# Kernel optimization log

Measured on AMD Instinct MI355X. Metric: run time of the kernel, lower is better.

## Reference

```python
import jax, jax.numpy as jnp
import numpy as np
import math

G, H, C_IN, C_QK, C_VAL, C_OUT = 12, 8, 64, 32, 32, 64
ROPE_BASE = 10000.0


def platonic_linear(x, W):
    # x: [B, N, G*ci]; W: [G, co, ci] group-shared weights.
    # Equivariant linear via (cyclic stand-in) Cayley table: out[g] = sum_g' W[(g'-g)%G] x[g']
    B, N, _ = x.shape
    co, ci = W.shape[1], W.shape[2]
    idx = (jnp.arange(G)[None, :] - jnp.arange(G)[:, None]) % G  # [G_out, G_in]
    Wfull = W[idx]  # [G, G, co, ci]
    xg = x.reshape(B, N, G, ci)
    out = jnp.einsum('bngi,hgoi->bnho', xg, Wfull)
    return out.reshape(B, N, G * co)


def rms_norm(x, w):
    eps = jnp.finfo(x.dtype).eps
    var = jnp.mean(x * x, axis=-1, keepdims=True)
    return x * jax.lax.rsqrt(var + eps) * w


def rotate_pairs(x, cos, sin):
    # interleaved pair rotation; x: [..., d], cos/sin: [..., d//2]
    x1, x2 = x[..., ::2], x[..., 1::2]
    o1 = x1 * cos - x2 * sin
    o2 = x1 * sin + x2 * cos
    return jnp.stack([o1, o2], axis=-1).reshape(x.shape)


def sequence_rope(x, pos):
    # x: [B, N, GH, c_qk]; pos: [B, N] int
    half = C_QK // 2
    inv_freq = ROPE_BASE ** (-jnp.arange(0, half, dtype=jnp.float32) / half)
    ang = pos.astype(jnp.float32)[..., None] * inv_freq  # [B, N, half]
    cos, sin = jnp.cos(ang)[:, :, None, :], jnp.sin(ang)[:, :, None, :]
    return rotate_pairs(x, cos, sin)


def z_rotations():
    # stand-in group rotations: z-axis rotations by 2*pi*g/G, [G, 3, 3]
    th = 2.0 * jnp.pi * jnp.arange(G, dtype=jnp.float32) / G
    c, s, z, o = jnp.cos(th), jnp.sin(th), jnp.zeros(G), jnp.ones(G)
    R = jnp.stack([c, -s, z, s, c, z, z, z, o], axis=-1).reshape(G, 3, 3)
    return R


def platonic_rope(x, coords, freqs):
    # x: [B, N, G, H, c_qk]; coords: [B, N, 3]; freqs: [H, c_qk//2, 3]
    R = z_rotations()
    phase = jnp.einsum('bnd,gde,hfe->bnghf', coords, R, freqs)  # [B,N,G,H,half]
    return rotate_pairs(x, jnp.cos(phase), jnp.sin(phase))


def setup_inputs() -> dict:
    key = jax.random.key(0)
    ks = jax.random.split(key, 10)
    B, N = 2, 512
    feat_Q = jax.random.normal(ks[0], (B, N, G * C_IN), dtype=jnp.float32)
    coords_Q = jax.random.normal(ks[1], (B, N, 3), dtype=jnp.float32)
    sequence_idxs = jnp.sort(jax.random.randint(ks[2], (B, N), 0, 2048), axis=-1).astype(jnp.int32)
    s_in = 1.0 / math.sqrt(G * C_IN)
    s_o = 1.0 / math.sqrt(G * H * C_VAL)
    Wq = jax.random.normal(ks[3], (G, H * C_QK, C_IN), dtype=jnp.float32) * s_in
    Wk = jax.random.normal(ks[4], (G, H * C_QK, C_IN), dtype=jnp.float32) * s_in
    Wv = jax.random.normal(ks[5], (G, H * C_VAL, C_IN), dtype=jnp.float32) * s_in
    Wo = jax.random.normal(ks[6], (G, C_OUT, H * C_VAL), dtype=jnp.float32) * s_o
    q_norm_w = jnp.ones((C_QK,), dtype=jnp.float32)
    k_norm_w = jnp.ones((C_QK,), dtype=jnp.float32)
    platonic_freqs = jax.random.normal(ks[7], (H, C_QK // 2, 3), dtype=jnp.float32)  # freq_sigma=1.0
    return dict(feat_Q=feat_Q, coords_Q=coords_Q, Wq=Wq, Wk=Wk, Wv=Wv, Wo=Wo,
                q_norm_w=q_norm_w, k_norm_w=k_norm_w, platonic_freqs=platonic_freqs,
                sequence_idxs=sequence_idxs)


def reference(feat_Q, coords_Q, Wq, Wk, Wv, Wo, q_norm_w, k_norm_w, platonic_freqs, sequence_idxs):
    B, NQ, _ = feat_Q.shape
    q = platonic_linear(feat_Q, Wq).reshape(B, NQ, G * H, C_QK)
    k = platonic_linear(feat_Q, Wk).reshape(B, NQ, G * H, C_QK)
    v = platonic_linear(feat_Q, Wv).reshape(B, NQ, G * H, C_VAL)
    q = rms_norm(q, q_norm_w)
    k = rms_norm(k, k_norm_w)
    q = sequence_rope(q, sequence_idxs)
    k = sequence_rope(k, sequence_idxs)
    q = platonic_rope(q.reshape(B, NQ, G, H, C_QK), coords_Q, platonic_freqs).reshape(B, NQ, G * H, C_QK)
    k = platonic_rope(k.reshape(B, NQ, G, H, C_QK), coords_Q, platonic_freqs).reshape(B, NQ, G * H, C_QK)
    # attention over G*H heads, scale 1/sqrt(c_qk) (as in SDPA)
    qh = q.transpose(0, 2, 1, 3)  # [B, GH, NQ, d]
    kh = k.transpose(0, 2, 1, 3)
    vh = v.transpose(0, 2, 1, 3)
    scores = jnp.einsum('bhqd,bhkd->bhqk', qh, kh) / math.sqrt(C_QK)
    attn = jax.nn.softmax(scores, axis=-1)
    out = jnp.einsum('bhqk,bhkd->bhqd', attn, vh)
    out = out.transpose(0, 2, 1, 3).reshape(B, NQ, G * H * C_VAL)
    return platonic_linear(out, Wo)
```

## Files before the change

### kernel.cpp

```cpp
#include <hip/hip_runtime.h>
#include <math.h>

#define NG   12
#define NH   8
#define CIN  64
#define CQK  32
#define CVAL 32
#define COUT 64
#define NB   2
#define NN   512
#define NROWS (NB * NN)
#define GHH  (NG * NH)
#define DIN  (NG * CIN)
#define DQK  (GHH * CQK)
#define DOUT (NG * COUT)

typedef __attribute__((ext_vector_type(8))) short bf16x8;
typedef __attribute__((ext_vector_type(4))) float f32x4;
typedef unsigned short ushort_t;

#define SZU ((size_t)NROWS * DQK)

__device__ __forceinline__ ushort_t bf16_rne(float v) {
    unsigned u = __float_as_uint(v);
    return (ushort_t)((u + 0x7fffu + ((u >> 16) & 1u)) >> 16);
}

__global__ __launch_bounds__(256) void prep_kernel(
    const float* __restrict__ feat,
    const float* __restrict__ Wq, const float* __restrict__ Wk,
    const float* __restrict__ Wv,
    ushort_t* __restrict__ Xrh, ushort_t* __restrict__ Xrl,
    ushort_t* __restrict__ Wqh, ushort_t* __restrict__ Wql)
{
    const int bb = blockIdx.x;
    if (bb < 384) {
        const int t  = bb * 256 + threadIdx.x;
        const int mr  = t & 15;
        const int u   = t >> 4;
        const int kc  = u % 96;
        const int m16 = u / 96;
        const float* src = feat + (size_t)(m16 * 16 + mr) * DIN + kc * 8;
        float v[8];
        *(float4*)v       = *(const float4*)src;
        *(float4*)(v + 4) = *(const float4*)(src + 4);
        ushort_t h8[8] __attribute__((aligned(16)));
        ushort_t l8[8] __attribute__((aligned(16)));
        #pragma unroll
        for (int j = 0; j < 8; ++j) {
            ushort_t hb = bf16_rne(v[j]);
            float hf = __uint_as_float(((unsigned)hb) << 16);
            h8[j] = hb;
            l8[j] = bf16_rne(v[j] - hf);
        }
        const size_t dst = ((size_t)m16 * 96 + kc) * 128 + mr * 8;
        *(uint4*)(Xrh + dst) = *(const uint4*)h8;
        *(uint4*)(Xrl + dst) = *(const uint4*)l8;
    } else {
        const int zz = (bb - 384) / 96;
        const float* W = (zz == 0) ? Wq : (zz == 1) ? Wk : Wv;
        ushort_t* hi = Wqh + (size_t)zz * 196608;
        ushort_t* lo = Wql + (size_t)zz * 196608;
        const int t  = ((bb - 384) % 96) * 256 + threadIdx.x;
        const int kc = t & 7;
        const int o  = (t >> 3) & 255;
        const int gp = t >> 11;
        const float* src = W + ((size_t)(gp * 256 + o)) * 64 + kc * 8;
        float v[8];
        *(float4*)v       = *(const float4*)src;
        *(float4*)(v + 4) = *(const float4*)(src + 4);
        ushort_t h8[8] __attribute__((aligned(16)));
        ushort_t l8[8] __attribute__((aligned(16)));
        #pragma unroll
        for (int j = 0; j < 8; ++j) {
            ushort_t hb = bf16_rne(v[j]);
            float hf = __uint_as_float(((unsigned)hb) << 16);
            h8[j] = hb;
            l8[j] = bf16_rne(v[j] - hf);
        }
        const size_t dst = ((size_t)(gp * 16 + (o >> 4)) * 8 + kc) * 128 + (o & 15) * 8;
        *(uint4*)(hi + dst) = *(const uint4*)h8;
        *(uint4*)(lo + dst) = *(const uint4*)l8;
    }
}

__global__ __launch_bounds__(256) void wo_swz_kernel(
    const float* __restrict__ Wo, ushort_t* __restrict__ hi,
    ushort_t* __restrict__ lo)
{
    const int t  = blockIdx.x * 256 + threadIdx.x;
    const int kc = t & 31;
    const int o  = (t >> 5) & 63;
    const int gp = t >> 11;
    const float* src = Wo + ((size_t)(gp * 64 + o)) * 256 + kc * 8;
    float v[8];
    *(float4*)v       = *(const float4*)src;
    *(float4*)(v + 4) = *(const float4*)(src + 4);
    ushort_t h8[8] __attribute__((aligned(16)));
    ushort_t l8[8] __attribute__((aligned(16)));
    #pragma unroll
    for (int j = 0; j < 8; ++j) {
        ushort_t hb = bf16_rne(v[j]);
        float hf = __uint_as_float(((unsigned)hb) << 16);
        h8[j] = hb;
        l8[j] = bf16_rne(v[j] - hf);
    }
    const size_t dst = ((size_t)(gp * 4 + (o >> 4)) * 32 + kc) * 128 + (o & 15) * 8;
    *(uint4*)(hi + dst) = *(const uint4*)h8;
    *(uint4*)(lo + dst) = *(const uint4*)l8;
}

__global__ __launch_bounds__(256, 1) void qkv_mfma_kernel(
    const ushort_t* __restrict__ Xrh, const ushort_t* __restrict__ Xrl,
    const ushort_t* __restrict__ Wrh, const ushort_t* __restrict__ Wrl,
    float* __restrict__ qo, float* __restrict__ ko, float* __restrict__ vo)
{
    const int z = blockIdx.z;
    float* __restrict__ out = (z == 0) ? qo : (z == 1) ? ko : vo;
    const ushort_t* Wh = Wrh + (size_t)z * 196608;
    const ushort_t* Wl = Wrl + (size_t)z * 196608;
    const int m0 = blockIdx.y * 128;
    const int c0 = blockIdx.x * 128;
    const int hg = c0 >> 8;
    const int o0 = c0 & 255;
    const int tid  = threadIdx.x;
    const int lane = tid & 63;
    const int w    = tid >> 6;
    const int wm   = (w >> 1) * 64;
    const int wn   = (w & 1) * 64;
    const int lm   = lane & 15;
    const int lq   = lane >> 4;
    const int tA0  = (m0 + wm) >> 4;
    const int ct0  = (o0 + wn) >> 4;

    f32x4 acc[4][4];
    #pragma unroll
    for (int i = 0; i < 4; ++i)
        #pragma unroll
        for (int j = 0; j < 4; ++j) acc[i][j] = (f32x4)(0.0f);

    for (int ks = 0; ks < 24; ++ks) {
        const int g = ks >> 1;
        int gp = g - hg; if (gp < 0) gp += NG;
        bf16x8 ah[4], al[4], bh[4], bl[4];
        #pragma unroll
        for (int mt = 0; mt < 4; ++mt) {
            const size_t aoff = ((size_t)(tA0 + mt) * 96 + ks * 4 + lq) * 128 + lm * 8;
            ah[mt] = *(const bf16x8*)(Xrh + aoff);
            al[mt] = *(const bf16x8*)(Xrl + aoff);
        }
        const size_t bbase = ((size_t)(gp * 16 + ct0) * 8 + (ks & 1) * 4 + lq) * 128 + lm * 8;
        #pragma unroll
        for (int nt = 0; nt < 4; ++nt) {
            bh[nt] = *(const bf16x8*)(Wh + bbase + nt * 1024);
            bl[nt] = *(const bf16x8*)(Wl + bbase + nt * 1024);
        }
        #pragma unroll
        for (int mt = 0; mt < 4; ++mt)
            #pragma unroll
            for (int nt = 0; nt < 4; ++nt) {
                acc[mt][nt] = __builtin_amdgcn_mfma_f32_16x16x32_bf16(ah[mt], bh[nt], acc[mt][nt], 0, 0, 0);
                acc[mt][nt] = __builtin_amdgcn_mfma_f32_16x16x32_bf16(ah[mt], bl[nt], acc[mt][nt], 0, 0, 0);
                acc[mt][nt] = __builtin_amdgcn_mfma_f32_16x16x32_bf16(al[mt], bh[nt], acc[mt][nt], 0, 0, 0);
            }
    }
    #pragma unroll
    for (int mt = 0; mt < 4; ++mt)
        #pragma unroll
        for (int r = 0; r < 4; ++r) {
            float* dst = out + (size_t)(m0 + wm + mt * 16 + lq * 4 + r) * DQK + c0 + wn + lm;
            #pragma unroll
            for (int nt = 0; nt < 4; ++nt) dst[nt * 16] = acc[mt][nt][r];
        }
}

__global__ __launch_bounds__(256) void norm_rope_kernel(
    float* __restrict__ q, const float* __restrict__ kin,
    ushort_t* __restrict__ krh, ushort_t* __restrict__ krl,
    const float* __restrict__ coords,
    const int* __restrict__ seq,
    const float* __restrict__ qw,
    const float* __restrict__ kw,
    const float* __restrict__ pf)
{
    const int hid = blockIdx.x * 256 + threadIdx.x;
    const int gh = hid % GHH;
    const int bn = hid / GHH;
    const int g = gh >> 3;
    const int h = gh & 7;
    float* qp = q + (size_t)hid * CQK;
    const float* kp = kin + (size_t)hid * CQK;
    float xq[CQK], xk[CQK];
    #pragma unroll
    for (int u = 0; u < 8; ++u) *(float4*)(xq + 4 * u) = *(const float4*)(qp + 4 * u);
    #pragma unroll
    for (int u = 0; u < 8; ++u) *(float4*)(xk + 4 * u) = *(const float4*)(kp + 4 * u);

    float sq = 0.f, sk = 0.f;
    #pragma unroll
    for (int c = 0; c < CQK; ++c) { sq = fmaf(xq[c], xq[c], sq); sk = fmaf(xk[c], xk[c], sk); }
    const float eps = 1.1920928955078125e-07f;
    const float invq = rsqrtf(sq * (1.f / CQK) + eps);
    const float invk = rsqrtf(sk * (1.f / CQK) + eps);
    #pragma unroll
    for (int c = 0; c < CQK; ++c) { xq[c] *= invq * qw[c]; xk[c] *= invk * kw[c]; }

    const float pos = (float)seq[bn];
    const float cx = coords[bn * 3 + 0], cy = coords[bn * 3 + 1], cz = coords[bn * 3 + 2];
    float sg, cg;
    sincosf((float)g * 0.5235987755982988f, &sg, &cg);
    const float u0 = cg * cx + sg * cy;
    const float u1 = cg * cy - sg * cx;
    const float u2 = cz;

    #pragma unroll
    for (int f = 0; f < 16; ++f) {
        const float invf = exp2f(-(float)f * 0.8304820237218405f);
        const float* fr = pf + ((size_t)h * 16 + f) * 3;
        const float ang = fmaf(pos, invf, u0 * fr[0] + u1 * fr[1] + u2 * fr[2]);
        float sn, cs;
        sincosf(ang, &sn, &cs);
        float a1 = xq[2 * f], a2 = xq[2 * f + 1];
        xq[2 * f]     = a1 * cs - a2 * sn;
        xq[2 * f + 1] = a1 * sn + a2 * cs;
        float b1 = xk[2 * f], b2 = xk[2 * f + 1];
        xk[2 * f]     = b1 * cs - b2 * sn;
        xk[2 * f + 1] = b1 * sn + b2 * cs;
    }
    #pragma unroll
    for (int u = 0; u < 8; ++u) *(float4*)(qp + 4 * u) = *(const float4*)(xq + 4 * u);

    const int b = bn >> 9, n = bn & 511;
    const size_t kbase = (((size_t)(b * GHH + gh) * 32 + (n >> 4)) * 4) * 128 + (n & 15) * 8;
    #pragma unroll
    for (int kc = 0; kc < 4; ++kc) {
        ushort_t h8[8] __attribute__((aligned(16)));
        ushort_t l8[8] __attribute__((aligned(16)));
        #pragma unroll
        for (int j = 0; j < 8; ++j) {
            const float x = xk[kc * 8 + j];
            const ushort_t hb = bf16_rne(x);
            h8[j] = hb;
            l8[j] = bf16_rne(x - __uint_as_float(((unsigned)hb) << 16));
        }
        *(uint4*)(krh + kbase + kc * 128) = *(const uint4*)h8;
        *(uint4*)(krl + kbase + kc * 128) = *(const uint4*)l8;
    }
}

__global__ __launch_bounds__(256) void vpack_kernel(
    const float* __restrict__ v,
    ushort_t* __restrict__ vrh, ushort_t* __restrict__ vrl)
{
    const int t  = blockIdx.x * 256 + threadIdx.x;
    const int vd = t & 31;
    const int kc = (t >> 5) & 63;
    const int bg = t >> 11;
    const int b  = (bg >= GHH) ? 1 : 0;
    const int gh = bg - b * GHH;
    const float* src = v + (size_t)(b * 512 + kc * 8) * DQK + gh * 32 + vd;
    ushort_t h8[8] __attribute__((aligned(16)));
    ushort_t l8[8] __attribute__((aligned(16)));
    #pragma unroll
    for (int j = 0; j < 8; ++j) {
        const float x = src[j * DQK];
        const ushort_t hb = bf16_rne(x);
        h8[j] = hb;
        l8[j] = bf16_rne(x - __uint_as_float(((unsigned)hb) << 16));
    }
    const size_t dst = ((size_t)(bg * 2 + (vd >> 4)) * 64 + kc) * 128 + (vd & 15) * 8;
    *(uint4*)(vrh + dst) = *(const uint4*)h8;
    *(uint4*)(vrl + dst) = *(const uint4*)l8;
}

__global__ __launch_bounds__(256, 1) void attn_mfma_kernel(
    const float* __restrict__ q,
    const ushort_t* __restrict__ krh, const ushort_t* __restrict__ krl,
    const ushort_t* __restrict__ vrh, const ushort_t* __restrict__ vrl,
    ushort_t* __restrict__ aoh,
    ushort_t* __restrict__ aol)
{
    __shared__ __attribute__((aligned(16))) ushort_t Ps[128][72];

    const int gh    = blockIdx.x;
    const int chunk = blockIdx.y;
    const int b     = blockIdx.z;
    const size_t headoff = (size_t)b * NN * DQK + (size_t)gh * CQK;
    const size_t kvhead = (size_t)(b * GHH + gh) * 16384;
    const int tid  = threadIdx.x;
    const int lane = tid & 63;
    const int w    = tid >> 6;
    const int lm   = lane & 15;
    const int lq   = lane >> 4;
    const int qloc = w * 32;

    const float scale = 0.17677669529663687f;
    bf16x8 qh[2], ql[2];
    #pragma unroll
    for (int mt = 0; mt < 2; ++mt) {
        const int row = chunk * 128 + qloc + mt * 16 + lm;
        const float* qp = q + headoff + (size_t)row * DQK + lq * 8;
        float4 t0 = *(const float4*)qp;
        float4 t1 = *(const float4*)(qp + 4);
        float vals[8] = {t0.x, t0.y, t0.z, t0.w, t1.x, t1.y, t1.z, t1.w};
        short h8[8], l8[8];
        #pragma unroll
        for (int j = 0; j < 8; ++j) {
            float x = vals[j] * scale;
            ushort_t hb = bf16_rne(x);
            float hf = __uint_as_float(((unsigned)hb) << 16);
            h8[j] = (short)hb;
            l8[j] = (short)bf16_rne(x - hf);
        }
        qh[mt] = *(bf16x8*)h8;
        ql[mt] = *(bf16x8*)l8;
    }

    float lacc[2][4];
    f32x4 o[2][2];
    #pragma unroll
    for (int mt = 0; mt < 2; ++mt) {
        #pragma unroll
        for (int r = 0; r < 4; ++r) lacc[mt][r] = 0.f;
        o[mt][0] = (f32x4)(0.0f); o[mt][1] = (f32x4)(0.0f);
    }

    for (int j0 = 0; j0 < NN; j0 += 64) {
        f32x4 sf[2][4];
        #pragma unroll
        for (int nt = 0; nt < 4; ++nt) {
            const size_t kb = kvhead + ((size_t)(((j0 >> 4) + nt) * 4 + lq)) * 128 + lm * 8;
            bf16x8 bh = *(const bf16x8*)(krh + kb);
            bf16x8 bl = *(const bf16x8*)(krl + kb);
            #pragma unroll
            for (int mt = 0; mt < 2; ++mt) {
                f32x4 s = (f32x4)(0.0f);
                s = __builtin_amdgcn_mfma_f32_16x16x32_bf16(qh[mt], bh, s, 0, 0, 0);
                s = __builtin_amdgcn_mfma_f32_16x16x32_bf16(qh[mt], bl, s, 0, 0, 0);
                s = __builtin_amdgcn_mfma_f32_16x16x32_bf16(ql[mt], bh, s, 0, 0, 0);
                sf[mt][nt] = s;
            }
        }

        #pragma unroll
        for (int mt = 0; mt < 2; ++mt)
            #pragma unroll
            for (int nt = 0; nt < 4; ++nt)
                #pragma unroll
                for (int r = 0; r < 4; ++r) {
                    const float p = __expf(sf[mt][nt][r]);
                    lacc[mt][r] += p;
                    Ps[qloc + mt * 16 + lq * 4 + r][nt * 16 + lm] = bf16_rne(p);
                }

        #pragma unroll
        for (int kt = 0; kt < 2; ++kt) {
            bf16x8 pa[2];
            #pragma unroll
            for (int mt = 0; mt < 2; ++mt)
                pa[mt] = *(const bf16x8*)&Ps[qloc + mt * 16 + lm][kt * 32 + lq * 8];
            #pragma unroll
            for (int vt = 0; vt < 2; ++vt) {
                const size_t vb = kvhead + ((size_t)(vt * 64 + (j0 >> 3) + kt * 4 + lq) * 16 + lm) * 8;
                bf16x8 bvh = *(const bf16x8*)(vrh + vb);
                bf16x8 bvl = *(const bf16x8*)(vrl + vb);
                #pragma unroll
                for (int mt = 0; mt < 2; ++mt) {
                    o[mt][vt] = __builtin_amdgcn_mfma_f32_16x16x32_bf16(pa[mt], bvh, o[mt][vt], 0, 0, 0);
                    o[mt][vt] = __builtin_amdgcn_mfma_f32_16x16x32_bf16(pa[mt], bvl, o[mt][vt], 0, 0, 0);
                }
            }
        }
    }

    #pragma unroll
    for (int mt = 0; mt < 2; ++mt)
        #pragma unroll
        for (int r = 0; r < 4; ++r) {
            float t = lacc[mt][r];
            t += __shfl_xor(t, 1, 64);
            t += __shfl_xor(t, 2, 64);
            t += __shfl_xor(t, 4, 64);
            t += __shfl_xor(t, 8, 64);
            lacc[mt][r] = 1.f / t;
        }

    const int mtbase = (b * 512 + chunk * 128 + qloc) >> 4;
    const int kc0 = gh * 4 + (lm >> 3);
    const int j0w = lm & 7;
    #pragma unroll
    for (int mt = 0; mt < 2; ++mt)
        #pragma unroll
        for (int r = 0; r < 4; ++r) {
            const size_t base = ((size_t)(mtbase + mt) * 384 + kc0) * 128 + (lq * 4 + r) * 8 + j0w;
            const float x0 = o[mt][0][r] * lacc[mt][r];
            const float x1 = o[mt][1][r] * lacc[mt][r];
            const ushort_t h0 = bf16_rne(x0);
            const ushort_t h1 = bf16_rne(x1);
            aoh[base]       = h0;
            aoh[base + 256] = h1;
            aol[base]       = bf16_rne(x0 - __uint_as_float(((unsigned)h0) << 16));
            aol[base + 256] = bf16_rne(x1 - __uint_as_float(((unsigned)h1) << 16));
        }
}

__global__ __launch_bounds__(256, 1) void oproj_mfma_kernel(
    const ushort_t* __restrict__ Arh, const ushort_t* __restrict__ Arl,
    const ushort_t* __restrict__ Worh, const ushort_t* __restrict__ Worl,
    float* __restrict__ part)
{
    const int h  = blockIdx.x;
    const int m0 = blockIdx.y * 128;
    const int kz = blockIdx.z;
    const int tid  = threadIdx.x;
    const int lane = tid & 63;
    const int w    = tid >> 6;
    const int wm   = (w >> 1) * 64;
    const int wn   = (w & 1) * 32;
    const int lm   = lane & 15;
    const int lq   = lane >> 4;
    const int tA0  = (m0 + wm) >> 4;
    const int ctb  = wn >> 4;

    f32x4 acc[4][2];
    #pragma unroll
    for (int i = 0; i < 4; ++i) { acc[i][0] = (f32x4)(0.0f); acc[i][1] = (f32x4)(0.0f); }

    for (int ks = 0; ks < 12; ++ks) {
        const int k0 = kz * 384 + ks * 32;
        const int g  = k0 >> 8;
        int gp = g - h; if (gp < 0) gp += NG;
        const int kcA = kz * 48 + ks * 4 + lq;
        const int kcB = ((k0 & 255) >> 3) + lq;
        bf16x8 ah[4], al[4], bh[2], bl[2];
        #pragma unroll
        for (int mt = 0; mt < 4; ++mt) {
            const size_t aoff = ((size_t)(tA0 + mt) * 384 + kcA) * 128 + lm * 8;
            ah[mt] = *(const bf16x8*)(Arh + aoff);
            al[mt] = *(const bf16x8*)(Arl + aoff);
        }
        const size_t bbase = ((size_t)(gp * 4 + ctb) * 32 + kcB) * 128 + lm * 8;
        #pragma unroll
        for (int nt = 0; nt < 2; ++nt) {
            bh[nt] = *(const bf16x8*)(Worh + bbase + nt * 4096);
            bl[nt] = *(const bf16x8*)(Worl + bbase + nt * 4096);
        }
        #pragma unroll
        for (int mt = 0; mt < 4; ++mt)
            #pragma unroll
            for (int nt = 0; nt < 2; ++nt) {
                acc[mt][nt] = __builtin_amdgcn_mfma_f32_16x16x32_bf16(ah[mt], bh[nt], acc[mt][nt], 0, 0, 0);
                acc[mt][nt] = __builtin_amdgcn_mfma_f32_16x16x32_bf16(ah[mt], bl[nt], acc[mt][nt], 0, 0, 0);
                acc[mt][nt] = __builtin_amdgcn_mfma_f32_16x16x32_bf16(al[mt], bh[nt], acc[mt][nt], 0, 0, 0);
            }
    }
    float* dst0 = part + (size_t)kz * (NROWS * DOUT);
    #pragma unroll
    for (int mt = 0; mt < 4; ++mt)
        #pragma unroll
        for (int r = 0; r < 4; ++r) {
            float* dst = dst0 + (size_t)(m0 + wm + mt * 16 + lq * 4 + r) * DOUT + h * 64 + wn + lm;
            dst[0]  = acc[mt][0][r];
            dst[16] = acc[mt][1][r];
        }
}

__global__ __launch_bounds__(256) void reduce8_kernel(
    const float* __restrict__ part, float* __restrict__ out)
{
    const int i = blockIdx.x * 256 + threadIdx.x;
    const float4* p = (const float4*)part;
    const int s = NROWS * DOUT / 4;
    float4 r = p[i];
    #pragma unroll
    for (int j = 1; j < 8; ++j) {
        float4 t = p[i + j * s];
        r.x += t.x; r.y += t.y; r.z += t.z; r.w += t.w;
    }
    ((float4*)out)[i] = r;
}

extern "C" void kernel_launch(void* const* d_in, const int* in_sizes, int n_in,
                              void* d_out, int out_size, void* d_ws, size_t ws_size,
                              hipStream_t stream)
{
    const float* feat   = (const float*)d_in[0];
    const float* coords = (const float*)d_in[1];
    const float* Wq     = (const float*)d_in[2];
    const float* Wk     = (const float*)d_in[3];
    const float* Wv     = (const float*)d_in[4];
    const float* Wo     = (const float*)d_in[5];
    const float* qw     = (const float*)d_in[6];
    const float* kw     = (const float*)d_in[7];
    const float* pf     = (const float*)d_in[8];
    const int*   seq    = (const int*)d_in[9];

    float* qreg  = (float*)d_ws;
    float* kreg  = qreg + SZU;
    float* vreg  = kreg + SZU;
    float* aoreg = vreg + SZU;

    ushort_t* Xrh = (ushort_t*)aoreg;
    ushort_t* Xrl = Xrh + (size_t)NROWS * DIN;
    ushort_t* Wqh = Xrl + (size_t)NROWS * DIN;
    ushort_t* Wql = Wqh + (size_t)3 * 196608;
    ushort_t* Krh = (ushort_t*)aoreg;
    ushort_t* Krl = Krh + SZU;
    ushort_t* Vrh = (ushort_t*)kreg;
    ushort_t* Vrl = Vrh + SZU;
    ushort_t* AOrh = (ushort_t*)vreg;
    ushort_t* AOrl = AOrh + SZU;
    ushort_t* WOrh = (ushort_t*)aoreg;
    ushort_t* WOrl = WOrh + (size_t)196608;
    float*    part = (float*)d_ws;

    prep_kernel<<<dim3(672), 256, 0, stream>>>(feat, Wq, Wk, Wv, Xrh, Xrl, Wqh, Wql);
    qkv_mfma_kernel<<<dim3(24, 8, 3), 256, 0, stream>>>(Xrh, Xrl, Wqh, Wql, qreg, kreg, vreg);
    norm_rope_kernel<<<dim3(384), 256, 0, stream>>>(qreg, kreg, Krh, Krl, coords, seq, qw, kw, pf);
    vpack_kernel<<<dim3(1536), 256, 0, stream>>>(vreg, Vrh, Vrl);
    attn_mfma_kernel<<<dim3(96, 4, 2), 256, 0, stream>>>(qreg, Krh, Krl, Vrh, Vrl, AOrh, AOrl);

    wo_swz_kernel<<<dim3(96), 256, 0, stream>>>(Wo, WOrh, WOrl);
    oproj_mfma_kernel<<<dim3(12, 8, 8), 256, 0, stream>>>(AOrh, AOrl, WOrh, WOrl, part);
    reduce8_kernel<<<dim3(768), 256, 0, stream>>>(part, (float*)d_out);
}
```

Before: 210.7 us.

## Halve QKV GEMM tile width and double-buffer fragment loads across k-steps

The QKV projection kernel now uses 128x64 output tiles instead of 128x128, which doubles the grid to 48x8x3 blocks, and raises launch bounds to allow two blocks per CU. The k-loop is fully unrolled with two register sets, so the next k-step's global loads are issued before the current step's MFMAs. This aims to hide global-load latency and improve occupancy and CU coverage. The cost is more total A-operand traffic, since each row tile is reloaded by twice as many blocks, and higher register pressure from the double buffers.

```diff
diff --git a/kernel.cpp b/kernel.cpp
--- a/kernel.cpp
+++ b/kernel.cpp
@@ -110,7 +110,7 @@
     *(uint4*)(lo + dst) = *(const uint4*)l8;
 }
 
-__global__ __launch_bounds__(256, 1) void qkv_mfma_kernel(
+__global__ __launch_bounds__(256, 2) void qkv_mfma_kernel(
     const ushort_t* __restrict__ Xrh, const ushort_t* __restrict__ Xrl,
     const ushort_t* __restrict__ Wrh, const ushort_t* __restrict__ Wrl,
     float* __restrict__ qo, float* __restrict__ ko, float* __restrict__ vo)
@@ -120,57 +120,78 @@
     const ushort_t* Wh = Wrh + (size_t)z * 196608;
     const ushort_t* Wl = Wrl + (size_t)z * 196608;
     const int m0 = blockIdx.y * 128;
-    const int c0 = blockIdx.x * 128;
+    const int c0 = blockIdx.x * 64;
     const int hg = c0 >> 8;
     const int o0 = c0 & 255;
     const int tid  = threadIdx.x;
     const int lane = tid & 63;
     const int w    = tid >> 6;
     const int wm   = (w >> 1) * 64;
-    const int wn   = (w & 1) * 64;
+    const int wn   = (w & 1) * 32;
     const int lm   = lane & 15;
     const int lq   = lane >> 4;
     const int tA0  = (m0 + wm) >> 4;
     const int ct0  = (o0 + wn) >> 4;
 
-    f32x4 acc[4][4];
-    #pragma unroll
-    for (int i = 0; i < 4; ++i)
-        #pragma unroll
-        for (int j = 0; j < 4; ++j) acc[i][j] = (f32x4)(0.0f);
-
-    for (int ks = 0; ks < 24; ++ks) {
-        const int g = ks >> 1;
-        int gp = g - hg; if (gp < 0) gp += NG;
-        bf16x8 ah[4], al[4], bh[4], bl[4];
-        #pragma unroll
-        for (int mt = 0; mt < 4; ++mt) {
-            const size_t aoff = ((size_t)(tA0 + mt) * 96 + ks * 4 + lq) * 128 + lm * 8;
-            ah[mt] = *(const bf16x8*)(Xrh + aoff);
-            al[mt] = *(const bf16x8*)(Xrl + aoff);
-        }
-        const size_t bbase = ((size_t)(gp * 16 + ct0) * 8 + (ks & 1) * 4 + lq) * 128 + lm * 8;
-        #pragma unroll
-        for (int nt = 0; nt < 4; ++nt) {
-            bh[nt] = *(const bf16x8*)(Wh + bbase + nt * 1024);
-            bl[nt] = *(const bf16x8*)(Wl + bbase + nt * 1024);
-        }
-        #pragma unroll
-        for (int mt = 0; mt < 4; ++mt)
-            #pragma unroll
-            for (int nt = 0; nt < 4; ++nt) {
-                acc[mt][nt] = __builtin_amdgcn_mfma_f32_16x16x32_bf16(ah[mt], bh[nt], acc[mt][nt], 0, 0, 0);
-                acc[mt][nt] = __builtin_amdgcn_mfma_f32_16x16x32_bf16(ah[mt], bl[nt], acc[mt][nt], 0, 0, 0);
-                acc[mt][nt] = __builtin_amdgcn_mfma_f32_16x16x32_bf16(al[mt], bh[nt], acc[mt][nt], 0, 0, 0);
-            }
-    }
+    f32x4 acc[4][2];
+    #pragma unroll
+    for (int i = 0; i < 4; ++i) { acc[i][0] = (f32x4)(0.0f); acc[i][1] = (f32x4)(0.0f); }
+
+#define LOADF(KS, AH, AL, BH, BL) do {                                          \
+        const int g_ = (KS) >> 1;                                               \
+        int gp_ = g_ - hg; if (gp_ < 0) gp_ += NG;                              \
+        _Pragma("unroll")                                                       \
+        for (int mt = 0; mt < 4; ++mt) {                                        \
+            const size_t aoff = ((size_t)(tA0 + mt) * 96 + (KS) * 4 + lq) * 128 \
+                                + lm * 8;                                       \
+            AH[mt] = *(const bf16x8*)(Xrh + aoff);                              \
+            AL[mt] = *(const bf16x8*)(Xrl + aoff);                              \
+        }                                                                       \
+        const size_t bb_ = ((size_t)(gp_ * 16 + ct0) * 8 + ((KS) & 1) * 4 + lq) \
+                           * 128 + lm * 8;                                      \
+        _Pragma("unroll")                                                       \
+        for (int nt = 0; nt < 2; ++nt) {                                        \
+            BH[nt] = *(const bf16x8*)(Wh + bb_ + nt * 1024);                    \
+            BL[nt] = *(const bf16x8*)(Wl + bb_ + nt * 1024);                    \
+        }                                                                       \
+    } while (0)
+
+#define MFMAS(AH, AL, BH, BL) do {                                              \
+        _Pragma("unroll")                                                       \
+        for (int mt = 0; mt < 4; ++mt)                                          \
+            _Pragma("unroll")                                                   \
+            for (int nt = 0; nt < 2; ++nt) {                                    \
+                acc[mt][nt] = __builtin_amdgcn_mfma_f32_16x16x32_bf16(          \
+                    AH[mt], BH[nt], acc[mt][nt], 0, 0, 0);                      \
+                acc[mt][nt] = __builtin_amdgcn_mfma_f32_16x16x32_bf16(          \
+                    AH[mt], BL[nt], acc[mt][nt], 0, 0, 0);                      \
+                acc[mt][nt] = __builtin_amdgcn_mfma_f32_16x16x32_bf16(          \
+                    AL[mt], BH[nt], acc[mt][nt], 0, 0, 0);                      \
+            }                                                                   \
+    } while (0)
+
+    bf16x8 ah0[4], al0[4], bh0[2], bl0[2];
+    bf16x8 ah1[4], al1[4], bh1[2], bl1[2];
+    LOADF(0, ah0, al0, bh0, bl0);
+    #pragma unroll
+    for (int ks = 0; ks < 24; ks += 2) {
+        LOADF(ks + 1, ah1, al1, bh1, bl1);
+        MFMAS(ah0, al0, bh0, bl0);
+        if (ks + 2 < 24) {
+            LOADF(ks + 2, ah0, al0, bh0, bl0);
+        }
+        MFMAS(ah1, al1, bh1, bl1);
+    }
+#undef LOADF
+#undef MFMAS
+
     #pragma unroll
     for (int mt = 0; mt < 4; ++mt)
         #pragma unroll
         for (int r = 0; r < 4; ++r) {
             float* dst = out + (size_t)(m0 + wm + mt * 16 + lq * 4 + r) * DQK + c0 + wn + lm;
-            #pragma unroll
-            for (int nt = 0; nt < 4; ++nt) dst[nt * 16] = acc[mt][nt][r];
+            dst[0]  = acc[mt][0][r];
+            dst[16] = acc[mt][1][r];
         }
 }
 
@@ -515,7 +536,7 @@
     float*    part = (float*)d_ws;
 
     prep_kernel<<<dim3(672), 256, 0, stream>>>(feat, Wq, Wk, Wv, Xrh, Xrl, Wqh, Wql);
-    qkv_mfma_kernel<<<dim3(24, 8, 3), 256, 0, stream>>>(Xrh, Xrl, Wqh, Wql, qreg, kreg, vreg);
+    qkv_mfma_kernel<<<dim3(48, 8, 3), 256, 0, stream>>>(Xrh, Xrl, Wqh, Wql, qreg, kreg, vreg);
     norm_rope_kernel<<<dim3(384), 256, 0, stream>>>(qreg, kreg, Krh, Krl, coords, seq, qw, kw, pf);
     vpack_kernel<<<dim3(1536), 256, 0, stream>>>(vreg, Vrh, Vrl);
     attn_mfma_kernel<<<dim3(96, 4, 2), 256, 0, stream>>>(qreg, Krh, Krl, Vrh, Vrl, AOrh, AOrl);
```

After: 247.1 us. +17.3%, slower.

## Fuse RMS norm, RoPE and K/V bf16 split-packing into QKV GEMM epilogue

Applied to the files above, without the earlier changes.

The QKV MFMA kernel's epilogue now does the RMS norm (a shuffle reduction across lanes), the sequence and platonic rotary embedding, and the hi/lo bf16 packing of K and V directly from the accumulators. This removes the separate norm_rope and vpack kernels along with the fp32 K/V round trip through global memory. Workspace buffers are reassigned so the new layout does not overlap live data. In exchange, the epilogue issues scattered 2-byte stores for K/V, repeats sincos per element, and adds register pressure to a kernel launched with one block per SIMD.

```diff
diff --git a/kernel.cpp b/kernel.cpp
--- a/kernel.cpp
+++ b/kernel.cpp
@@ -113,10 +113,14 @@
 __global__ __launch_bounds__(256, 1) void qkv_mfma_kernel(
     const ushort_t* __restrict__ Xrh, const ushort_t* __restrict__ Xrl,
     const ushort_t* __restrict__ Wrh, const ushort_t* __restrict__ Wrl,
-    float* __restrict__ qo, float* __restrict__ ko, float* __restrict__ vo)
+    float* __restrict__ qo,
+    ushort_t* __restrict__ krh, ushort_t* __restrict__ krl,
+    ushort_t* __restrict__ vrh, ushort_t* __restrict__ vrl,
+    const float* __restrict__ coords, const int* __restrict__ seq,
+    const float* __restrict__ qw, const float* __restrict__ kw,
+    const float* __restrict__ pf)
 {
     const int z = blockIdx.z;
-    float* __restrict__ out = (z == 0) ? qo : (z == 1) ? ko : vo;
     const ushort_t* Wh = Wrh + (size_t)z * 196608;
     const ushort_t* Wl = Wrl + (size_t)z * 196608;
     const int m0 = blockIdx.y * 128;
@@ -164,113 +168,97 @@
                 acc[mt][nt] = __builtin_amdgcn_mfma_f32_16x16x32_bf16(al[mt], bh[nt], acc[mt][nt], 0, 0, 0);
             }
     }
+
+    if (z == 2) {
+        #pragma unroll
+        for (int mt = 0; mt < 4; ++mt)
+            #pragma unroll
+            for (int r = 0; r < 4; ++r) {
+                const int row = m0 + wm + mt * 16 + lq * 4 + r;
+                const int b   = row >> 9, key = row & 511;
+                #pragma unroll
+                for (int nt = 0; nt < 4; ++nt) {
+                    const int col = c0 + wn + nt * 16 + lm;
+                    const int gh  = col >> 5, vd = col & 31;
+                    const size_t dst = ((size_t)((b * GHH + gh) * 2 + (vd >> 4)) * 64
+                                        + (key >> 3)) * 128 + (vd & 15) * 8 + (key & 7);
+                    const float x = acc[mt][nt][r];
+                    const ushort_t hb = bf16_rne(x);
+                    vrh[dst] = hb;
+                    vrl[dst] = bf16_rne(x - __uint_as_float(((unsigned)hb) << 16));
+                }
+            }
+        return;
+    }
+
+    const float eps = 1.1920928955078125e-07f;
+    const float* nw = (z == 0) ? qw : kw;
+    const float wA = nw[lm];
+    const float wB = nw[lm + 16];
+    const int   fA = lm >> 1;
+    const int   fB = 8 + (lm >> 1);
+    const float invfA = exp2f(-(float)fA * 0.8304820237218405f);
+    const float invfB = exp2f(-(float)fB * 0.8304820237218405f);
+    const int gh0 = (c0 + wn) >> 5;
+    float sgp[2], cgp[2], frA[2][3], frB[2][3];
+    #pragma unroll
+    for (int p = 0; p < 2; ++p) {
+        const int ghp = gh0 + p;
+        sincosf((float)(ghp >> 3) * 0.5235987755982988f, &sgp[p], &cgp[p]);
+        const int h = ghp & 7;
+        #pragma unroll
+        for (int e = 0; e < 3; ++e) {
+            frA[p][e] = pf[((size_t)h * 16 + fA) * 3 + e];
+            frB[p][e] = pf[((size_t)h * 16 + fB) * 3 + e];
+        }
+    }
+    const float psign = (lm & 1) ? 1.0f : -1.0f;
+
     #pragma unroll
     for (int mt = 0; mt < 4; ++mt)
         #pragma unroll
         for (int r = 0; r < 4; ++r) {
-            float* dst = out + (size_t)(m0 + wm + mt * 16 + lq * 4 + r) * DQK + c0 + wn + lm;
-            #pragma unroll
-            for (int nt = 0; nt < 4; ++nt) dst[nt * 16] = acc[mt][nt][r];
-        }
-}
-
-__global__ __launch_bounds__(256) void norm_rope_kernel(
-    float* __restrict__ q, const float* __restrict__ kin,
-    ushort_t* __restrict__ krh, ushort_t* __restrict__ krl,
-    const float* __restrict__ coords,
-    const int* __restrict__ seq,
-    const float* __restrict__ qw,
-    const float* __restrict__ kw,
-    const float* __restrict__ pf)
-{
-    const int hid = blockIdx.x * 256 + threadIdx.x;
-    const int gh = hid % GHH;
-    const int bn = hid / GHH;
-    const int g = gh >> 3;
-    const int h = gh & 7;
-    float* qp = q + (size_t)hid * CQK;
-    const float* kp = kin + (size_t)hid * CQK;
-    float xq[CQK], xk[CQK];
-    #pragma unroll
-    for (int u = 0; u < 8; ++u) *(float4*)(xq + 4 * u) = *(const float4*)(qp + 4 * u);
-    #pragma unroll
-    for (int u = 0; u < 8; ++u) *(float4*)(xk + 4 * u) = *(const float4*)(kp + 4 * u);
-
-    float sq = 0.f, sk = 0.f;
-    #pragma unroll
-    for (int c = 0; c < CQK; ++c) { sq = fmaf(xq[c], xq[c], sq); sk = fmaf(xk[c], xk[c], sk); }
-    const float eps = 1.1920928955078125e-07f;
-    const float invq = rsqrtf(sq * (1.f / CQK) + eps);
-    const float invk = rsqrtf(sk * (1.f / CQK) + eps);
-    #pragma unroll
-    for (int c = 0; c < CQK; ++c) { xq[c] *= invq * qw[c]; xk[c] *= invk * kw[c]; }
-
-    const float pos = (float)seq[bn];
-    const float cx = coords[bn * 3 + 0], cy = coords[bn * 3 + 1], cz = coords[bn * 3 + 2];
-    float sg, cg;
-    sincosf((float)g * 0.5235987755982988f, &sg, &cg);
-    const float u0 = cg * cx + sg * cy;
-    const float u1 = cg * cy - sg * cx;
-    const float u2 = cz;
-
-    #pragma unroll
-    for (int f = 0; f < 16; ++f) {
-        const float invf = exp2f(-(float)f * 0.8304820237218405f);
-        const float* fr = pf + ((size_t)h * 16 + f) * 3;
-        const float ang = fmaf(pos, invf, u0 * fr[0] + u1 * fr[1] + u2 * fr[2]);
-        float sn, cs;
-        sincosf(ang, &sn, &cs);
-        float a1 = xq[2 * f], a2 = xq[2 * f + 1];
-        xq[2 * f]     = a1 * cs - a2 * sn;
-        xq[2 * f + 1] = a1 * sn + a2 * cs;
-        float b1 = xk[2 * f], b2 = xk[2 * f + 1];
-        xk[2 * f]     = b1 * cs - b2 * sn;
-        xk[2 * f + 1] = b1 * sn + b2 * cs;
-    }
-    #pragma unroll
-    for (int u = 0; u < 8; ++u) *(float4*)(qp + 4 * u) = *(const float4*)(xq + 4 * u);
-
-    const int b = bn >> 9, n = bn & 511;
-    const size_t kbase = (((size_t)(b * GHH + gh) * 32 + (n >> 4)) * 4) * 128 + (n & 15) * 8;
-    #pragma unroll
-    for (int kc = 0; kc < 4; ++kc) {
-        ushort_t h8[8] __attribute__((aligned(16)));
-        ushort_t l8[8] __attribute__((aligned(16)));
-        #pragma unroll
-        for (int j = 0; j < 8; ++j) {
-            const float x = xk[kc * 8 + j];
-            const ushort_t hb = bf16_rne(x);
-            h8[j] = hb;
-            l8[j] = bf16_rne(x - __uint_as_float(((unsigned)hb) << 16));
-        }
-        *(uint4*)(krh + kbase + kc * 128) = *(const uint4*)h8;
-        *(uint4*)(krl + kbase + kc * 128) = *(const uint4*)l8;
-    }
-}
-
-__global__ __launch_bounds__(256) void vpack_kernel(
-    const float* __restrict__ v,
-    ushort_t* __restrict__ vrh, ushort_t* __restrict__ vrl)
-{
-    const int t  = blockIdx.x * 256 + threadIdx.x;
-    const int vd = t & 31;
-    const int kc = (t >> 5) & 63;
-    const int bg = t >> 11;
-    const int b  = (bg >= GHH) ? 1 : 0;
-    const int gh = bg - b * GHH;
-    const float* src = v + (size_t)(b * 512 + kc * 8) * DQK + gh * 32 + vd;
-    ushort_t h8[8] __attribute__((aligned(16)));
-    ushort_t l8[8] __attribute__((aligned(16)));
-    #pragma unroll
-    for (int j = 0; j < 8; ++j) {
-        const float x = src[j * DQK];
-        const ushort_t hb = bf16_rne(x);
-        h8[j] = hb;
-        l8[j] = bf16_rne(x - __uint_as_float(((unsigned)hb) << 16));
-    }
-    const size_t dst = ((size_t)(bg * 2 + (vd >> 4)) * 64 + kc) * 128 + (vd & 15) * 8;
-    *(uint4*)(vrh + dst) = *(const uint4*)h8;
-    *(uint4*)(vrl + dst) = *(const uint4*)l8;
+            const int row = m0 + wm + mt * 16 + lq * 4 + r;
+            const float pos = (float)seq[row];
+            const float cx = coords[row * 3], cy = coords[row * 3 + 1], cz = coords[row * 3 + 2];
+            #pragma unroll
+            for (int p = 0; p < 2; ++p) {
+                float ss = acc[mt][2 * p][r] * acc[mt][2 * p][r]
+                         + acc[mt][2 * p + 1][r] * acc[mt][2 * p + 1][r];
+                ss += __shfl_xor(ss, 1, 64);
+                ss += __shfl_xor(ss, 2, 64);
+                ss += __shfl_xor(ss, 4, 64);
+                ss += __shfl_xor(ss, 8, 64);
+                const float inv = rsqrtf(ss * (1.0f / 32.0f) + eps);
+                const float u0 = cgp[p] * cx + sgp[p] * cy;
+                const float u1 = cgp[p] * cy - sgp[p] * cx;
+                const float u2 = cz;
+                #pragma unroll
+                for (int par = 0; par < 2; ++par) {
+                    const int nt = 2 * p + par;
+                    const float x   = acc[mt][nt][r] * inv * (par ? wB : wA);
+                    const float prt = __shfl_xor(x, 1, 64);
+                    const float* fr = par ? frB[p] : frA[p];
+                    const float ang = fmaf(pos, par ? invfB : invfA,
+                                           u0 * fr[0] + u1 * fr[1] + u2 * fr[2]);
+                    float sn, cs;
+                    sincosf(ang, &sn, &cs);
+                    const float o = x * cs + prt * sn * psign;
+                    if (z == 0) {
+                        qo[(size_t)row * DQK + c0 + wn + nt * 16 + lm] = o;
+                    } else {
+                        const int b = row >> 9, n = row & 511;
+                        const int gh = gh0 + p;
+                        const int d  = par * 16 + lm;
+                        const size_t dst = (((size_t)(b * GHH + gh) * 32 + (n >> 4)) * 4
+                                            + (d >> 3)) * 128 + (n & 15) * 8 + (d & 7);
+                        const ushort_t hb = bf16_rne(o);
+                        krh[dst] = hb;
+                        krl[dst] = bf16_rne(o - __uint_as_float(((unsigned)hb) << 16));
+                    }
+                }
+            }
+        }
 }
 
 __global__ __launch_bounds__(256, 1) void attn_mfma_kernel(
@@ -504,20 +492,19 @@
     ushort_t* Xrl = Xrh + (size_t)NROWS * DIN;
     ushort_t* Wqh = Xrl + (size_t)NROWS * DIN;
     ushort_t* Wql = Wqh + (size_t)3 * 196608;
-    ushort_t* Krh = (ushort_t*)aoreg;
+    ushort_t* Krh = (ushort_t*)kreg;
     ushort_t* Krl = Krh + SZU;
-    ushort_t* Vrh = (ushort_t*)kreg;
+    ushort_t* Vrh = (ushort_t*)vreg;
     ushort_t* Vrl = Vrh + SZU;
-    ushort_t* AOrh = (ushort_t*)vreg;
+    ushort_t* AOrh = (ushort_t*)aoreg;
     ushort_t* AOrl = AOrh + SZU;
-    ushort_t* WOrh = (ushort_t*)aoreg;
+    ushort_t* WOrh = (ushort_t*)qreg;
     ushort_t* WOrl = WOrh + (size_t)196608;
-    float*    part = (float*)d_ws;
+    float*    part = (float*)kreg;
 
     prep_kernel<<<dim3(672), 256, 0, stream>>>(feat, Wq, Wk, Wv, Xrh, Xrl, Wqh, Wql);
-    qkv_mfma_kernel<<<dim3(24, 8, 3), 256, 0, stream>>>(Xrh, Xrl, Wqh, Wql, qreg, kreg, vreg);
-    norm_rope_kernel<<<dim3(384), 256, 0, stream>>>(qreg, kreg, Krh, Krl, coords, seq, qw, kw, pf);
-    vpack_kernel<<<dim3(1536), 256, 0, stream>>>(vreg, Vrh, Vrl);
+    qkv_mfma_kernel<<<dim3(24, 8, 3), 256, 0, stream>>>(Xrh, Xrl, Wqh, Wql,
+        qreg, Krh, Krl, Vrh, Vrl, coords, seq, qw, kw, pf);
     attn_mfma_kernel<<<dim3(96, 4, 2), 256, 0, stream>>>(qreg, Krh, Krl, Vrh, Vrl, AOrh, AOrl);
 
     wo_swz_kernel<<<dim3(96), 256, 0, stream>>>(Wo, WOrh, WOrl);
```

Result: no change. 214.9 us (+2.0%).
